# Kernel optimization log

Hardware: AMD Instinct MI355X
Metric: run time of the kernel (lower is better)

## Reference

```python
import jax, jax.numpy as jnp
import numpy as np


def setup_inputs() -> dict:
    key = jax.random.key(0)
    kx, kq, kk, kv = jax.random.split(key, 4)
    d_model, d_head = 1024, 64
    x = jax.random.normal(kx, (4, 4096, d_model), dtype=jnp.float32)
    scale = 1.0 / np.sqrt(d_model)
    Wq = jax.random.normal(kq, (d_model, d_head), dtype=jnp.float32) * scale
    Wk = jax.random.normal(kk, (d_model, d_head), dtype=jnp.float32) * scale
    Wv = jax.random.normal(kv, (d_model, d_head), dtype=jnp.float32) * scale
    return {"x": x, "Wq": Wq, "Wk": Wk, "Wv": Wv}


def reference(x, Wq, Wk, Wv):
    # x: [B, S, D]; Wq/Wk/Wv: [D, H]
    d_head = Wq.shape[-1]
    Q = jnp.einsum('bsd,dh->bsh', x, Wq)
    K = jnp.einsum('bsd,dh->bsh', x, Wk)
    V = jnp.einsum('bsd,dh->bsh', x, Wv)
    scores = jnp.einsum('bqh,bkh->bqk', Q, K) / jnp.sqrt(jnp.float32(d_head))
    S = x.shape[1]
    causal = jnp.tril(jnp.ones((S, S), dtype=bool))  # [S, S]
    scores = jnp.where(causal, scores, -jnp.inf)
    weights = jax.nn.softmax(scores, axis=-1)  # [B, S, S]
    return jnp.einsum('bqk,bkh->bqh', weights, V)
```

## Files before the change

kernel.cpp:

```cpp
#include <hip/hip_runtime.h>

#define D_MODEL 1024
#define D_HEAD  64
#define SEQ     4096
#define BATCH   4
#define M_TOT   (BATCH * SEQ)
#define LOG2E   1.44269504088896f
#define MFIX_L2 17.3123404906676f
#define CHUNK   4

typedef __bf16 bf16;
typedef bf16  bf16x8 __attribute__((ext_vector_type(8)));
typedef float f32x4  __attribute__((ext_vector_type(4)));

#define MFMA(a, b, c) __builtin_amdgcn_mfma_f32_16x16x32_bf16(a, b, c, 0, 0, 0)

#define QKV_OFF  0
#define OBUF_OFF 6291456
#define LBUF_OFF 10485760
#define WT_OFF   10551296
#define VT_OFF   10944512

__global__ void prep_kernel(const float* __restrict__ Wq, const float* __restrict__ Wk,
                            const float* __restrict__ Wv, bf16* __restrict__ Wt,
                            float4* __restrict__ zp, int n4)
{
    const int bx = blockIdx.x;
    const int t  = threadIdx.x;
    if (bx < 48) {
        __shared__ bf16 tr[64][72];
        const int wm = bx >> 4, kt = bx & 15, k0 = kt * 64;
        const float* W = (wm == 0) ? Wq : (wm == 1) ? Wk : Wv;
        const int kr = t >> 2, nb = (t & 3) * 16;
        #pragma unroll
        for (int j = 0; j < 4; j++) {
            float4 wrow = *(const float4*)(W + (size_t)(k0 + kr) * D_HEAD + nb + j * 4);
            tr[nb + j * 4 + 0][kr] = (bf16)wrow.x;
            tr[nb + j * 4 + 1][kr] = (bf16)wrow.y;
            tr[nb + j * 4 + 2][kr] = (bf16)wrow.z;
            tr[nb + j * 4 + 3][kr] = (bf16)wrow.w;
        }
        __syncthreads();
        const int n = t >> 2, kc = (t & 3) * 8;
        bf16* dst = Wt + (size_t)(wm * 64 + n) * D_MODEL + k0;
        #pragma unroll
        for (int h = 0; h < 2; h++) {
            bf16x8 v;
            #pragma unroll
            for (int j = 0; j < 8; j++) v[j] = tr[n][kc + h * 32 + j];
            *(bf16x8*)(dst + kc + h * 32) = v;
        }
    } else {
        int i = (bx - 48) * 256 + t;
        if (i < n4) zp[i] = float4{0.f, 0.f, 0.f, 0.f};
    }
}

#define XP 40

__global__ __launch_bounds__(512) void proj_kernel(
    const float* __restrict__ x, const bf16* __restrict__ Wt,
    bf16* __restrict__ qkv)
{
    __shared__ __align__(16) bf16 xs[2][2][64][XP];
    __shared__ __align__(16) bf16 ws[2][2][192][XP];
    __shared__ float red[64][193];

    const int t    = threadIdx.x;
    const int w    = t >> 6;
    const int g    = w >> 2;
    const int nw   = w & 3;
    const int lane = t & 63;
    const int quad = lane >> 4;
    const int l15  = lane & 15;
    const int row0 = blockIdx.x * 64;
    const int kb   = g * 512;

    const int tg   = t & 255;
    const int xrow = tg >> 2, xkq = (tg & 3) * 8;

    const float* xg = x + (size_t)(row0 + xrow) * D_MODEL + kb + xkq;

    f32x4 acc[12] = {};

    float4 xa, xb;
    bf16x8 wtv[3];

    auto load_regs = [&](int c) {
        xa = *(const float4*)(xg + c * 32);
        xb = *(const float4*)(xg + c * 32 + 4);
        #pragma unroll
        for (int it = 0; it < 3; it++) {
            int id = tg + it * 256, n = id >> 2, kk8 = (id & 3) * 8;
            wtv[it] = *(const bf16x8*)(Wt + (size_t)n * D_MODEL + kb + c * 32 + kk8);
        }
    };
    auto store_lds = [&](int p) {
        bf16x8 xv;
        xv[0] = (bf16)xa.x; xv[1] = (bf16)xa.y; xv[2] = (bf16)xa.z; xv[3] = (bf16)xa.w;
        xv[4] = (bf16)xb.x; xv[5] = (bf16)xb.y; xv[6] = (bf16)xb.z; xv[7] = (bf16)xb.w;
        *(bf16x8*)&xs[p][g][xrow][xkq] = xv;
        #pragma unroll
        for (int it = 0; it < 3; it++) {
            int id = tg + it * 256, n = id >> 2, kk8 = (id & 3) * 8;
            *(bf16x8*)&ws[p][g][n][kk8] = wtv[it];
        }
    };

    load_regs(0);
    store_lds(0);
    load_regs(1);
    __syncthreads();

    int p = 0;
    for (int c = 0; c < 16; c++) {
        bf16x8 af[4], bfr[3];
        #pragma unroll
        for (int rg = 0; rg < 4; rg++)
            af[rg] = *(bf16x8*)&xs[p][g][rg * 16 + l15][quad * 8];
        #pragma unroll
        for (int j = 0; j < 3; j++)
            bfr[j] = *(bf16x8*)&ws[p][g][nw * 48 + j * 16 + l15][quad * 8];
        #pragma unroll
        for (int rg = 0; rg < 4; rg++)
            #pragma unroll
            for (int j = 0; j < 3; j++)
                acc[rg * 3 + j] = MFMA(af[rg], bfr[j], acc[rg * 3 + j]);

        if (c + 1 < 16) {
            store_lds(p ^ 1);
            if (c + 2 < 16) load_regs(c + 2);
        }
        __syncthreads();
        p ^= 1;
    }

    if (g == 1) {
        #pragma unroll
        for (int rg = 0; rg < 4; rg++)
            #pragma unroll
            for (int j = 0; j < 3; j++)
                #pragma unroll
                for (int r = 0; r < 4; r++)
                    red[rg * 16 + quad * 4 + r][nw * 48 + j * 16 + l15] =
                        acc[rg * 3 + j][r];
    }
    __syncthreads();
    if (g == 0) {
        #pragma unroll
        for (int rg = 0; rg < 4; rg++)
            #pragma unroll
            for (int j = 0; j < 3; j++) {
                const int col = nw * 48 + j * 16 + l15;
                const int wm = col >> 6, h = col & 63;
                const float sc = (wm == 0) ? 0.125f : 1.0f;
                bf16* outp = qkv + (size_t)wm * M_TOT * D_HEAD;
                #pragma unroll
                for (int r = 0; r < 4; r++) {
                    const int row = rg * 16 + quad * 4 + r;
                    float s = acc[rg * 3 + j][r] + red[row][col];
                    outp[(size_t)(row0 + row) * D_HEAD + h] = (bf16)(s * sc);
                }
            }
    }
}

__global__ void vtrans_kernel(const bf16* __restrict__ qkv, bf16* __restrict__ vt)
{
    __shared__ bf16 trs[64][72];
    const bf16* Vsec = qkv + (size_t)2 * M_TOT * D_HEAD;
    const int t  = threadIdx.x;
    const int m0 = blockIdx.x * 64;
    const int b  = m0 >> 12, s0 = m0 & (SEQ - 1);

    #pragma unroll
    for (int half = 0; half < 2; half++) {
        const int ml = (t >> 3) + half * 32, hc = t & 7;
        bf16x8 v = *(const bf16x8*)(Vsec + (size_t)(m0 + ml) * D_HEAD + hc * 8);
        #pragma unroll
        for (int j = 0; j < 8; j++) trs[hc * 8 + j][ml] = v[j];
    }
    __syncthreads();
    #pragma unroll
    for (int half = 0; half < 2; half++) {
        const int hl = (t >> 3) + half * 32, sc = t & 7;
        bf16x8 v;
        #pragma unroll
        for (int j = 0; j < 8; j++) v[j] = trs[hl][sc * 8 + j];
        *(bf16x8*)(vt + ((size_t)b * D_HEAD + hl) * SEQ + s0 + sc * 8) = v;
    }
}

#define TS 72

__global__ __launch_bounds__(256) void attn_kernel(
    const bf16* __restrict__ qkv, const bf16* __restrict__ vt,
    float* __restrict__ o_buf, float* __restrict__ l_buf)
{
    const int i = blockIdx.x;
    const int c = blockIdx.y;
    const int b = blockIdx.z;
    const int ntiles = i + 1;
    const int tile0  = c * CHUNK;
    if (tile0 >= ntiles) return;
    const int tile1 = min(tile0 + CHUNK, ntiles);

    __shared__ __align__(16) bf16 Ks[64][TS];
    __shared__ __align__(16) bf16 Vs[64][TS];
    __shared__ __align__(16) bf16 Ps[4][16][TS];

    const bf16* Q = qkv;
    const bf16* K = qkv + (size_t)M_TOT * D_HEAD;

    const int t    = threadIdx.x;
    const int wv   = t >> 6;
    const int lane = t & 63;
    const int quad = lane >> 4;
    const int l15  = lane & 15;
    const int qb   = i * 64;
    const size_t base  = (size_t)b * SEQ * D_HEAD;
    const bf16* vtb = vt + (size_t)b * D_HEAD * SEQ;

    bf16x8 qf0, qf1;
    {
        const bf16* qr = Q + base + (size_t)(qb + wv * 16 + l15) * D_HEAD;
        qf0 = *(const bf16x8*)(qr + quad * 8);
        qf1 = *(const bf16x8*)(qr + 32 + quad * 8);
    }

    f32x4 o[4] = {};
    float l_r[4] = {};
    const int qw0 = qb + wv * 16;

    const int dr  = t >> 2;
    const int kq8 = (t & 3) * 8;

    bf16x8 kr0, kr1, vr0, vr1;
    {
        const bf16* kp = K + base + (size_t)(tile0 * 64 + dr) * D_HEAD;
        kr0 = *(const bf16x8*)(kp + kq8);
        kr1 = *(const bf16x8*)(kp + kq8 + 32);
        const bf16* vp = vtb + (size_t)dr * SEQ + tile0 * 64;
        vr0 = *(const bf16x8*)(vp + kq8);
        vr1 = *(const bf16x8*)(vp + kq8 + 32);
    }

    for (int tile = tile0; tile < tile1; tile++) {
        const int kk0 = tile * 64;
        *(bf16x8*)&Ks[dr][kq8]      = kr0;
        *(bf16x8*)&Ks[dr][kq8 + 32] = kr1;
        *(bf16x8*)&Vs[dr][kq8]      = vr0;
        *(bf16x8*)&Vs[dr][kq8 + 32] = vr1;
        __syncthreads();

        if (tile + 1 < tile1) {
            const bf16* kp = K + base + (size_t)((tile + 1) * 64 + dr) * D_HEAD;
            kr0 = *(const bf16x8*)(kp + kq8);
            kr1 = *(const bf16x8*)(kp + kq8 + 32);
            const bf16* vp = vtb + (size_t)dr * SEQ + (tile + 1) * 64;
            vr0 = *(const bf16x8*)(vp + kq8);
            vr1 = *(const bf16x8*)(vp + kq8 + 32);
        }

        f32x4 sc4[4];
        #pragma unroll
        for (int kt = 0; kt < 4; kt++) {
            f32x4 z = {};
            z = MFMA(qf0, *(bf16x8*)&Ks[kt * 16 + l15][quad * 8],      z);
            z = MFMA(qf1, *(bf16x8*)&Ks[kt * 16 + l15][32 + quad * 8], z);
            sc4[kt] = z;
        }

        const bool need_mask = (tile == i);

        #pragma unroll
        for (int r = 0; r < 4; r++) {
            #pragma unroll
            for (int kt = 0; kt < 4; kt++) {
                float s = sc4[kt][r];
                if (need_mask && (kk0 + kt * 16 + l15 > qw0 + quad * 4 + r))
                    s = -1e30f;
                float p = __builtin_amdgcn_exp2f(fmaf(s, LOG2E, -MFIX_L2));
                l_r[r] += p;
                Ps[wv][quad * 4 + r][kt * 16 + l15] = (bf16)p;
            }
        }
        __syncthreads();

        #pragma unroll
        for (int c2 = 0; c2 < 2; c2++) {
            bf16x8 pa = *(bf16x8*)&Ps[wv][l15][c2 * 32 + quad * 8];
            #pragma unroll
            for (int t4 = 0; t4 < 4; t4++) {
                bf16x8 vb = *(bf16x8*)&Vs[t4 * 16 + l15][c2 * 32 + quad * 8];
                o[t4] = MFMA(pa, vb, o[t4]);
            }
        }
        __syncthreads();
    }

    const int mrow0 = b * SEQ + qw0;
    #pragma unroll
    for (int r = 0; r < 4; r++) {
        float ls = l_r[r];
        #pragma unroll
        for (int sh = 1; sh < 16; sh <<= 1)
            ls += __shfl_xor(ls, sh, 64);
        if (l15 == 0)
            atomicAdd(&l_buf[mrow0 + quad * 4 + r], ls);
        const size_t orow = (size_t)(mrow0 + quad * 4 + r) * D_HEAD;
        #pragma unroll
        for (int t4 = 0; t4 < 4; t4++)
            atomicAdd(&o_buf[orow + t4 * 16 + l15], o[t4][r]);
    }
}

__global__ void norm_kernel(const float4* __restrict__ o_buf,
                            const float* __restrict__ l_buf,
                            float4* __restrict__ out)
{
    int gid = blockIdx.x * 256 + threadIdx.x;
    int m = gid >> 4;
    float inv = 1.0f / l_buf[m];
    float4 v = o_buf[gid];
    out[gid] = float4{v.x * inv, v.y * inv, v.z * inv, v.w * inv};
}

extern "C" void kernel_launch(void* const* d_in, const int* in_sizes, int n_in,
                              void* d_out, int out_size, void* d_ws, size_t ws_size,
                              hipStream_t stream) {
    const float* x  = (const float*)d_in[0];
    const float* Wq = (const float*)d_in[1];
    const float* Wk = (const float*)d_in[2];
    const float* Wv = (const float*)d_in[3];

    bf16*  qkv   = (bf16*)((char*)d_ws + QKV_OFF);
    float* o_buf = (float*)((char*)d_ws + OBUF_OFF);
    float* l_buf = (float*)((char*)d_ws + LBUF_OFF);
    bf16*  Wt    = (bf16*)((char*)d_ws + WT_OFF);
    bf16*  vt    = (bf16*)((char*)d_ws + VT_OFF);

    const int zero4 = (M_TOT * 65) / 4;
    const int zblocks = (zero4 + 255) / 256;
    prep_kernel<<<48 + zblocks, 256, 0, stream>>>(Wq, Wk, Wv, Wt,
                                                  (float4*)o_buf, zero4);
    proj_kernel<<<M_TOT / 64, 512, 0, stream>>>(x, Wt, qkv);
    vtrans_kernel<<<M_TOT / 64, 256, 0, stream>>>(qkv, vt);
    attn_kernel<<<dim3(SEQ / 64, SEQ / 64 / CHUNK, BATCH), 256, 0, stream>>>(
        qkv, vt, o_buf, l_buf);
    norm_kernel<<<M_TOT * 16 / 256, 256, 0, stream>>>((const float4*)o_buf, l_buf,
                                                      (float4*)d_out);
}
```

Measured before the change: 160.6 us.

## Switch attention to 32x32 MFMA tiles with 128-query blocks

The attention kernel now uses the 32x32x16 bf16 MFMA instead of 16x16x32, so each wave handles 32 query rows and each block handles 128 queries. Every K/V tile staged in shared memory is therefore reused across twice as many queries, which halves K/V global traffic and the number of partial-sum atomics per key chunk. The barrier between writing the probability tile and the PV product is dropped, because each wave only reads its own slice of Ps. The costs are higher register use (16-element accumulators and 16 row sums), some wasted exp and MFMA work on fully masked diagonal tiles for lower waves, and a coarser grid.

```diff
diff --git a/kernel.cpp b/kernel.cpp
--- a/kernel.cpp
+++ b/kernel.cpp
@@ -10,10 +10,12 @@
 #define CHUNK   4
 
 typedef __bf16 bf16;
-typedef bf16  bf16x8 __attribute__((ext_vector_type(8)));
-typedef float f32x4  __attribute__((ext_vector_type(4)));
-
-#define MFMA(a, b, c) __builtin_amdgcn_mfma_f32_16x16x32_bf16(a, b, c, 0, 0, 0)
+typedef bf16  bf16x8  __attribute__((ext_vector_type(8)));
+typedef float f32x4   __attribute__((ext_vector_type(4)));
+typedef float f32x16  __attribute__((ext_vector_type(16)));
+
+#define MFMA(a, b, c)   __builtin_amdgcn_mfma_f32_16x16x32_bf16(a, b, c, 0, 0, 0)
+#define MFMA32(a, b, c) __builtin_amdgcn_mfma_f32_32x32x16_bf16(a, b, c, 0, 0, 0)
 
 #define QKV_OFF  0
 #define OBUF_OFF 6291456
@@ -200,14 +202,14 @@
     const int i = blockIdx.x;
     const int c = blockIdx.y;
     const int b = blockIdx.z;
-    const int ntiles = i + 1;
+    const int ntiles = 2 * i + 2;
     const int tile0  = c * CHUNK;
     if (tile0 >= ntiles) return;
     const int tile1 = min(tile0 + CHUNK, ntiles);
 
     __shared__ __align__(16) bf16 Ks[64][TS];
     __shared__ __align__(16) bf16 Vs[64][TS];
-    __shared__ __align__(16) bf16 Ps[4][16][TS];
+    __shared__ __align__(16) bf16 Ps[4][32][TS];
 
     const bf16* Q = qkv;
     const bf16* K = qkv + (size_t)M_TOT * D_HEAD;
@@ -215,22 +217,23 @@
     const int t    = threadIdx.x;
     const int wv   = t >> 6;
     const int lane = t & 63;
-    const int quad = lane >> 4;
-    const int l15  = lane & 15;
-    const int qb   = i * 64;
-    const size_t base  = (size_t)b * SEQ * D_HEAD;
+    const int l31  = lane & 31;
+    const int kh   = lane >> 5;
+    const int qb   = i * 128;
+    const size_t base = (size_t)b * SEQ * D_HEAD;
     const bf16* vtb = vt + (size_t)b * D_HEAD * SEQ;
 
-    bf16x8 qf0, qf1;
+    bf16x8 qf[4];
     {
-        const bf16* qr = Q + base + (size_t)(qb + wv * 16 + l15) * D_HEAD;
-        qf0 = *(const bf16x8*)(qr + quad * 8);
-        qf1 = *(const bf16x8*)(qr + 32 + quad * 8);
-    }
-
-    f32x4 o[4] = {};
-    float l_r[4] = {};
-    const int qw0 = qb + wv * 16;
+        const bf16* qr = Q + base + (size_t)(qb + wv * 32 + l31) * D_HEAD;
+        #pragma unroll
+        for (int kc = 0; kc < 4; kc++)
+            qf[kc] = *(const bf16x8*)(qr + kc * 16 + kh * 8);
+    }
+
+    f32x16 o0 = {}, o1 = {};
+    float l_r[16] = {};
+    const int qw0 = qb + wv * 32;
 
     const int dr  = t >> 2;
     const int kq8 = (t & 3) * 8;
@@ -262,56 +265,52 @@
             vr1 = *(const bf16x8*)(vp + kq8 + 32);
         }
 
-        f32x4 sc4[4];
-        #pragma unroll
-        for (int kt = 0; kt < 4; kt++) {
-            f32x4 z = {};
-            z = MFMA(qf0, *(bf16x8*)&Ks[kt * 16 + l15][quad * 8],      z);
-            z = MFMA(qf1, *(bf16x8*)&Ks[kt * 16 + l15][32 + quad * 8], z);
-            sc4[kt] = z;
-        }
-
-        const bool need_mask = (tile == i);
-
-        #pragma unroll
-        for (int r = 0; r < 4; r++) {
-            #pragma unroll
-            for (int kt = 0; kt < 4; kt++) {
-                float s = sc4[kt][r];
-                if (need_mask && (kk0 + kt * 16 + l15 > qw0 + quad * 4 + r))
-                    s = -1e30f;
-                float p = __builtin_amdgcn_exp2f(fmaf(s, LOG2E, -MFIX_L2));
-                l_r[r] += p;
-                Ps[wv][quad * 4 + r][kt * 16 + l15] = (bf16)p;
+        const bool need_mask = (kk0 + 63 > qw0);
+
+        #pragma unroll
+        for (int kb = 0; kb < 2; kb++) {
+            f32x16 s16 = {};
+            #pragma unroll
+            for (int kc = 0; kc < 4; kc++) {
+                bf16x8 bk = *(bf16x8*)&Ks[kb * 32 + l31][kc * 16 + kh * 8];
+                s16 = MFMA32(qf[kc], bk, s16);
             }
-        }
-        __syncthreads();
-
-        #pragma unroll
-        for (int c2 = 0; c2 < 2; c2++) {
-            bf16x8 pa = *(bf16x8*)&Ps[wv][l15][c2 * 32 + quad * 8];
-            #pragma unroll
-            for (int t4 = 0; t4 < 4; t4++) {
-                bf16x8 vb = *(bf16x8*)&Vs[t4 * 16 + l15][c2 * 32 + quad * 8];
-                o[t4] = MFMA(pa, vb, o[t4]);
+            const int key = kk0 + kb * 32 + l31;
+            #pragma unroll
+            for (int reg = 0; reg < 16; reg++) {
+                const int row = (reg & 3) + 8 * (reg >> 2) + 4 * kh;
+                float s = s16[reg];
+                if (need_mask && (key > qw0 + row)) s = -1e30f;
+                float pv = __builtin_amdgcn_exp2f(fmaf(s, LOG2E, -MFIX_L2));
+                l_r[reg] += pv;
+                Ps[wv][row][kb * 32 + l31] = (bf16)pv;
             }
+        }
+
+        #pragma unroll
+        for (int kc = 0; kc < 4; kc++) {
+            bf16x8 pa = *(bf16x8*)&Ps[wv][l31][kc * 16 + kh * 8];
+            bf16x8 vb0 = *(bf16x8*)&Vs[l31][kc * 16 + kh * 8];
+            bf16x8 vb1 = *(bf16x8*)&Vs[32 + l31][kc * 16 + kh * 8];
+            o0 = MFMA32(pa, vb0, o0);
+            o1 = MFMA32(pa, vb1, o1);
         }
         __syncthreads();
     }
 
     const int mrow0 = b * SEQ + qw0;
     #pragma unroll
-    for (int r = 0; r < 4; r++) {
-        float ls = l_r[r];
-        #pragma unroll
-        for (int sh = 1; sh < 16; sh <<= 1)
+    for (int reg = 0; reg < 16; reg++) {
+        const int row = (reg & 3) + 8 * (reg >> 2) + 4 * kh;
+        float ls = l_r[reg];
+        #pragma unroll
+        for (int sh = 1; sh < 32; sh <<= 1)
             ls += __shfl_xor(ls, sh, 64);
-        if (l15 == 0)
-            atomicAdd(&l_buf[mrow0 + quad * 4 + r], ls);
-        const size_t orow = (size_t)(mrow0 + quad * 4 + r) * D_HEAD;
-        #pragma unroll
-        for (int t4 = 0; t4 < 4; t4++)
-            atomicAdd(&o_buf[orow + t4 * 16 + l15], o[t4][r]);
+        if (l31 == 0)
+            atomicAdd(&l_buf[mrow0 + row], ls);
+        const size_t orow = (size_t)(mrow0 + row) * D_HEAD;
+        atomicAdd(&o_buf[orow + l31],      o0[reg]);
+        atomicAdd(&o_buf[orow + 32 + l31], o1[reg]);
     }
 }
 
@@ -346,7 +345,7 @@
                                                   (float4*)o_buf, zero4);
     proj_kernel<<<M_TOT / 64, 512, 0, stream>>>(x, Wt, qkv);
     vtrans_kernel<<<M_TOT / 64, 256, 0, stream>>>(qkv, vt);
-    attn_kernel<<<dim3(SEQ / 64, SEQ / 64 / CHUNK, BATCH), 256, 0, stream>>>(
+    attn_kernel<<<dim3(SEQ / 128, 16, BATCH), 256, 0, stream>>>(
         qkv, vt, o_buf, l_buf);
     norm_kernel<<<M_TOT * 16 / 256, 256, 0, stream>>>((const float4*)o_buf, l_buf,
                                                       (float4*)d_out);
```

After: 181.7 us. +13.2%, slower.

## Fuse V transpose into projection, fold normalization into attention, drop split-K

Applied to the files above, without the earlier changes.

The projection kernel drops its two-group split-K and LDS reduction and now runs 256 threads per block over the full K range. Its epilogue writes V directly in transposed layout, which removes the separate vtrans kernel. The attention kernel uses a per-query-tile atomic counter so the last chunk block normalizes O by l and writes the output, replacing norm_kernel; the counter is zeroed together with the accumulators. One __syncthreads between the per-wave P write and its read is removed. The trade-offs are less parallelism inside each projection block, scattered 2-byte transposed stores of V, and extra fence and atomic overhead at the end of every attention block.

```diff
diff --git a/kernel.cpp b/kernel.cpp
--- a/kernel.cpp
+++ b/kernel.cpp
@@ -18,8 +18,9 @@
 #define QKV_OFF  0
 #define OBUF_OFF 6291456
 #define LBUF_OFF 10485760
-#define WT_OFF   10551296
-#define VT_OFF   10944512
+#define CNT_OFF  10551296
+#define WT_OFF   10552320
+#define VT_OFF   10945536
 
 __global__ void prep_kernel(const float* __restrict__ Wq, const float* __restrict__ Wk,
                             const float* __restrict__ Wv, bf16* __restrict__ Wt,
@@ -58,28 +59,22 @@
 
 #define XP 40
 
-__global__ __launch_bounds__(512) void proj_kernel(
+__global__ __launch_bounds__(256, 4) void proj_kernel(
     const float* __restrict__ x, const bf16* __restrict__ Wt,
-    bf16* __restrict__ qkv)
+    bf16* __restrict__ qkv, bf16* __restrict__ vt)
 {
-    __shared__ __align__(16) bf16 xs[2][2][64][XP];
-    __shared__ __align__(16) bf16 ws[2][2][192][XP];
-    __shared__ float red[64][193];
+    __shared__ __align__(16) bf16 xs[2][64][XP];
+    __shared__ __align__(16) bf16 ws[2][192][XP];
 
     const int t    = threadIdx.x;
-    const int w    = t >> 6;
-    const int g    = w >> 2;
-    const int nw   = w & 3;
+    const int nw   = t >> 6;
     const int lane = t & 63;
     const int quad = lane >> 4;
     const int l15  = lane & 15;
     const int row0 = blockIdx.x * 64;
-    const int kb   = g * 512;
-
-    const int tg   = t & 255;
-    const int xrow = tg >> 2, xkq = (tg & 3) * 8;
-
-    const float* xg = x + (size_t)(row0 + xrow) * D_MODEL + kb + xkq;
+
+    const int xrow = t >> 2, xkq = (t & 3) * 8;
+    const float* xg = x + (size_t)(row0 + xrow) * D_MODEL + xkq;
 
     f32x4 acc[12] = {};
 
@@ -91,19 +86,19 @@
         xb = *(const float4*)(xg + c * 32 + 4);
         #pragma unroll
         for (int it = 0; it < 3; it++) {
-            int id = tg + it * 256, n = id >> 2, kk8 = (id & 3) * 8;
-            wtv[it] = *(const bf16x8*)(Wt + (size_t)n * D_MODEL + kb + c * 32 + kk8);
+            int id = t + it * 256, n = id >> 2, kk8 = (id & 3) * 8;
+            wtv[it] = *(const bf16x8*)(Wt + (size_t)n * D_MODEL + c * 32 + kk8);
         }
     };
     auto store_lds = [&](int p) {
         bf16x8 xv;
         xv[0] = (bf16)xa.x; xv[1] = (bf16)xa.y; xv[2] = (bf16)xa.z; xv[3] = (bf16)xa.w;
         xv[4] = (bf16)xb.x; xv[5] = (bf16)xb.y; xv[6] = (bf16)xb.z; xv[7] = (bf16)xb.w;
-        *(bf16x8*)&xs[p][g][xrow][xkq] = xv;
+        *(bf16x8*)&xs[p][xrow][xkq] = xv;
         #pragma unroll
         for (int it = 0; it < 3; it++) {
-            int id = tg + it * 256, n = id >> 2, kk8 = (id & 3) * 8;
-            *(bf16x8*)&ws[p][g][n][kk8] = wtv[it];
+            int id = t + it * 256, n = id >> 2, kk8 = (id & 3) * 8;
+            *(bf16x8*)&ws[p][n][kk8] = wtv[it];
         }
     };
 
@@ -113,89 +108,57 @@
     __syncthreads();
 
     int p = 0;
-    for (int c = 0; c < 16; c++) {
+    for (int c = 0; c < 32; c++) {
         bf16x8 af[4], bfr[3];
         #pragma unroll
         for (int rg = 0; rg < 4; rg++)
-            af[rg] = *(bf16x8*)&xs[p][g][rg * 16 + l15][quad * 8];
+            af[rg] = *(bf16x8*)&xs[p][rg * 16 + l15][quad * 8];
         #pragma unroll
         for (int j = 0; j < 3; j++)
-            bfr[j] = *(bf16x8*)&ws[p][g][nw * 48 + j * 16 + l15][quad * 8];
+            bfr[j] = *(bf16x8*)&ws[p][nw * 48 + j * 16 + l15][quad * 8];
         #pragma unroll
         for (int rg = 0; rg < 4; rg++)
             #pragma unroll
             for (int j = 0; j < 3; j++)
                 acc[rg * 3 + j] = MFMA(af[rg], bfr[j], acc[rg * 3 + j]);
 
-        if (c + 1 < 16) {
+        if (c + 1 < 32) {
             store_lds(p ^ 1);
-            if (c + 2 < 16) load_regs(c + 2);
-        }
-        __syncthreads();
-        p ^= 1;
-    }
-
-    if (g == 1) {
-        #pragma unroll
-        for (int rg = 0; rg < 4; rg++)
-            #pragma unroll
-            for (int j = 0; j < 3; j++)
-                #pragma unroll
-                for (int r = 0; r < 4; r++)
-                    red[rg * 16 + quad * 4 + r][nw * 48 + j * 16 + l15] =
-                        acc[rg * 3 + j][r];
-    }
-    __syncthreads();
-    if (g == 0) {
-        #pragma unroll
-        for (int rg = 0; rg < 4; rg++)
-            #pragma unroll
-            for (int j = 0; j < 3; j++) {
-                const int col = nw * 48 + j * 16 + l15;
-                const int wm = col >> 6, h = col & 63;
-                const float sc = (wm == 0) ? 0.125f : 1.0f;
-                bf16* outp = qkv + (size_t)wm * M_TOT * D_HEAD;
-                #pragma unroll
-                for (int r = 0; r < 4; r++) {
-                    const int row = rg * 16 + quad * 4 + r;
-                    float s = acc[rg * 3 + j][r] + red[row][col];
-                    outp[(size_t)(row0 + row) * D_HEAD + h] = (bf16)(s * sc);
+            if (c + 2 < 32) load_regs(c + 2);
+            __syncthreads();
+            p ^= 1;
+        }
+    }
+
+    const int bb = row0 >> 12, ss = row0 & (SEQ - 1);
+    #pragma unroll
+    for (int rg = 0; rg < 4; rg++)
+        #pragma unroll
+        for (int j = 0; j < 3; j++) {
+            const int col = nw * 48 + j * 16 + l15;
+            const int wm = col >> 6, h = col & 63;
+            #pragma unroll
+            for (int r = 0; r < 4; r++) {
+                const int row = rg * 16 + quad * 4 + r;
+                const float v = acc[rg * 3 + j][r];
+                if (wm == 0) {
+                    qkv[(size_t)(row0 + row) * D_HEAD + h] = (bf16)(v * 0.125f);
+                } else if (wm == 1) {
+                    qkv[(size_t)M_TOT * D_HEAD +
+                        (size_t)(row0 + row) * D_HEAD + h] = (bf16)v;
+                } else {
+                    vt[((size_t)bb * D_HEAD + h) * SEQ + ss + row] = (bf16)v;
                 }
             }
-    }
-}
-
-__global__ void vtrans_kernel(const bf16* __restrict__ qkv, bf16* __restrict__ vt)
-{
-    __shared__ bf16 trs[64][72];
-    const bf16* Vsec = qkv + (size_t)2 * M_TOT * D_HEAD;
-    const int t  = threadIdx.x;
-    const int m0 = blockIdx.x * 64;
-    const int b  = m0 >> 12, s0 = m0 & (SEQ - 1);
-
-    #pragma unroll
-    for (int half = 0; half < 2; half++) {
-        const int ml = (t >> 3) + half * 32, hc = t & 7;
-        bf16x8 v = *(const bf16x8*)(Vsec + (size_t)(m0 + ml) * D_HEAD + hc * 8);
-        #pragma unroll
-        for (int j = 0; j < 8; j++) trs[hc * 8 + j][ml] = v[j];
-    }
-    __syncthreads();
-    #pragma unroll
-    for (int half = 0; half < 2; half++) {
-        const int hl = (t >> 3) + half * 32, sc = t & 7;
-        bf16x8 v;
-        #pragma unroll
-        for (int j = 0; j < 8; j++) v[j] = trs[hl][sc * 8 + j];
-        *(bf16x8*)(vt + ((size_t)b * D_HEAD + hl) * SEQ + s0 + sc * 8) = v;
-    }
+        }
 }
 
 #define TS 72
 
 __global__ __launch_bounds__(256) void attn_kernel(
     const bf16* __restrict__ qkv, const bf16* __restrict__ vt,
-    float* __restrict__ o_buf, float* __restrict__ l_buf)
+    float* __restrict__ o_buf, float* __restrict__ l_buf,
+    int* __restrict__ cnt, float* __restrict__ out)
 {
     const int i = blockIdx.x;
     const int c = blockIdx.y;
@@ -208,6 +171,7 @@
     __shared__ __align__(16) bf16 Ks[64][TS];
     __shared__ __align__(16) bf16 Vs[64][TS];
     __shared__ __align__(16) bf16 Ps[4][16][TS];
+    __shared__ int lastflag;
 
     const bf16* Q = qkv;
     const bf16* K = qkv + (size_t)M_TOT * D_HEAD;
@@ -218,7 +182,7 @@
     const int quad = lane >> 4;
     const int l15  = lane & 15;
     const int qb   = i * 64;
-    const size_t base  = (size_t)b * SEQ * D_HEAD;
+    const size_t base = (size_t)b * SEQ * D_HEAD;
     const bf16* vtb = vt + (size_t)b * D_HEAD * SEQ;
 
     bf16x8 qf0, qf1;
@@ -280,12 +244,11 @@
                 float s = sc4[kt][r];
                 if (need_mask && (kk0 + kt * 16 + l15 > qw0 + quad * 4 + r))
                     s = -1e30f;
-                float p = __builtin_amdgcn_exp2f(fmaf(s, LOG2E, -MFIX_L2));
-                l_r[r] += p;
-                Ps[wv][quad * 4 + r][kt * 16 + l15] = (bf16)p;
+                float pv = __builtin_amdgcn_exp2f(fmaf(s, LOG2E, -MFIX_L2));
+                l_r[r] += pv;
+                Ps[wv][quad * 4 + r][kt * 16 + l15] = (bf16)pv;
             }
         }
-        __syncthreads();
 
         #pragma unroll
         for (int c2 = 0; c2 < 2; c2++) {
@@ -313,17 +276,27 @@
         for (int t4 = 0; t4 < 4; t4++)
             atomicAdd(&o_buf[orow + t4 * 16 + l15], o[t4][r]);
     }
-}
-
-__global__ void norm_kernel(const float4* __restrict__ o_buf,
-                            const float* __restrict__ l_buf,
-                            float4* __restrict__ out)
-{
-    int gid = blockIdx.x * 256 + threadIdx.x;
-    int m = gid >> 4;
-    float inv = 1.0f / l_buf[m];
-    float4 v = o_buf[gid];
-    out[gid] = float4{v.x * inv, v.y * inv, v.z * inv, v.w * inv};
+
+    __threadfence();
+    if (t == 0) {
+        const int expected = (i + CHUNK) / CHUNK;
+        const int prev = atomicAdd(&cnt[b * (SEQ / 64) + i], 1);
+        lastflag = (prev == expected - 1);
+    }
+    __syncthreads();
+    if (lastflag) {
+        __threadfence();
+        const size_t f40 = (size_t)(b * SEQ + qb) * 16;
+        const float4* ob = (const float4*)o_buf + f40;
+        float4*       op = (float4*)out + f40;
+        #pragma unroll
+        for (int j = 0; j < 4; j++) {
+            const int idx = t + j * 256;
+            const float inv = 1.0f / l_buf[b * SEQ + qb + (idx >> 4)];
+            float4 v = ob[idx];
+            op[idx] = float4{v.x * inv, v.y * inv, v.z * inv, v.w * inv};
+        }
+    }
 }
 
 extern "C" void kernel_launch(void* const* d_in, const int* in_sizes, int n_in,
@@ -337,17 +310,15 @@
     bf16*  qkv   = (bf16*)((char*)d_ws + QKV_OFF);
     float* o_buf = (float*)((char*)d_ws + OBUF_OFF);
     float* l_buf = (float*)((char*)d_ws + LBUF_OFF);
+    int*   cnt   = (int*)((char*)d_ws + CNT_OFF);
     bf16*  Wt    = (bf16*)((char*)d_ws + WT_OFF);
     bf16*  vt    = (bf16*)((char*)d_ws + VT_OFF);
 
-    const int zero4 = (M_TOT * 65) / 4;
-    const int zblocks = (zero4 + 255) / 256;
+    const int n4 = (M_TOT * 65 * 4 + 256 * 4) / 16;
+    const int zblocks = (n4 + 255) / 256;
     prep_kernel<<<48 + zblocks, 256, 0, stream>>>(Wq, Wk, Wv, Wt,
-                                                  (float4*)o_buf, zero4);
-    proj_kernel<<<M_TOT / 64, 512, 0, stream>>>(x, Wt, qkv);
-    vtrans_kernel<<<M_TOT / 64, 256, 0, stream>>>(qkv, vt);
+                                                  (float4*)o_buf, n4);
+    proj_kernel<<<M_TOT / 64, 256, 0, stream>>>(x, Wt, qkv, vt);
     attn_kernel<<<dim3(SEQ / 64, SEQ / 64 / CHUNK, BATCH), 256, 0, stream>>>(
-        qkv, vt, o_buf, l_buf);
-    norm_kernel<<<M_TOT * 16 / 256, 256, 0, stream>>>((const float4*)o_buf, l_buf,
-                                                      (float4*)d_out);
+        qkv, vt, o_buf, l_buf, cnt, (float*)d_out);
 }
```

Result: slower. 368.0 us (+129.2%).
